# Optimization experiments

Hardware: AMD Instinct MI355X
Metric: run time of the kernel (lower is better)

The kernel has to match this reference:

```python
import jax, jax.numpy as jnp
import numpy as np

HEAD_NUM = 16
SCALE = 1.0 / np.sqrt(HEAD_NUM)  # source divides by sqrt(head_num), not head_dim
MASK_VAL = -10000000.0


def setup_inputs() -> dict:
    key = jax.random.key(0)
    kq, kk, kv = jax.random.split(key, 3)
    shape = (2, 16, 2048, 64)  # [B, H, L, D]
    Q = jax.random.normal(kq, shape, dtype=jnp.float32)
    K = jax.random.normal(kk, shape, dtype=jnp.float32)
    V = jax.random.normal(kv, shape, dtype=jnp.float32)
    return {"Q": Q, "K": K, "V": V}


def reference(Q, K, V):
    L = Q.shape[-2]
    # [B, H, L, M] attention logits, scaled by 1/sqrt(head_num)
    logits = jnp.einsum('bhld,bhmd->bhlm', Q, K) * SCALE
    # causal mask: strictly-upper triangle gets -1e7 (additive, as in source)
    mask = jnp.triu(jnp.ones((L, L), dtype=logits.dtype), 1) * MASK_VAL
    logits = logits + mask[None, None, :, :]
    weights = jax.nn.softmax(logits, axis=-1)
    return jnp.einsum('bhlm,bhmd->bhld', weights, V)
```

## Files before the change

### kernel.cpp

```cpp
#include <hip/hip_runtime.h>
#include <hip/hip_bf16.h>

#define BM 128
#define BN 64
#define HD 64
#define LQ 2048
#define SD 72

typedef __attribute__((ext_vector_type(8))) short short8;
typedef __attribute__((ext_vector_type(16))) float f32x16;

#define QSCALE 0.360673760222241f

static __device__ __forceinline__ unsigned pk2(float a, float b) {
    union { __hip_bfloat162 h2; unsigned u; } c;
    c.h2 = __float22bfloat162_rn(make_float2(a, b));
    return c.u;
}

__global__ __launch_bounds__(512, 4)
void fa_fwd(const float* __restrict__ Qg,
            const float* __restrict__ Kg,
            const float* __restrict__ Vg,
            float* __restrict__ Og) {
    __shared__ __align__(16) unsigned short lds[(2 * BN + 2 * HD) * SD];
    typedef unsigned short KT[BN][SD];
    typedef unsigned short VT[HD][SD];
    KT* sK  = (KT*)lds;
    VT* sVt = (VT*)(lds + 2 * BN * SD);

    const int t    = threadIdx.x;
    const int w    = t >> 6;
    const int lane = t & 63;
    const int h    = lane >> 5;
    const int l31  = lane & 31;
    const int qd   = lane >> 4;
    const int qg   = w & 3;
    const int kh   = w >> 2;

    const int bx  = blockIdx.x;
    const int idx = (bx >> 5) & 7;
    const int qt  = (bx & 256) ? idx : (15 - idx);
    const int bh  = bx & 31;
    const int q0  = qt * BM;

    const size_t base = (size_t)bh * (LQ * HD);
    const float* Qp = Qg + base + (size_t)q0 * HD;
    const float* Kp = Kg + base;
    const float* Vp = Vg + base;

    const int r0 = t >> 4;
    const int c4 = (t & 15) * 4;
    const int RA = w * 4;

    {
        unsigned short (*sQ)[SD] = (unsigned short (*)[SD])lds;
#pragma unroll
        for (int p = 0; p < 4; ++p) {
            const int r = p * 32 + r0;
            const float4 v = *(const float4*)(Qp + (size_t)r * HD + c4);
            uint2 u;
            u.x = pk2(v.x * QSCALE, v.y * QSCALE);
            u.y = pk2(v.z * QSCALE, v.w * QSCALE);
            *(uint2*)&sQ[r][c4] = u;
        }
    }
    __syncthreads();
    short8 qreg[4];
    {
        unsigned short (*sQ)[SD] = (unsigned short (*)[SD])lds;
#pragma unroll
        for (int ks = 0; ks < 4; ++ks)
            qreg[ks] = *(const short8*)&sQ[qg * 32 + l31][ks * 16 + h * 8];
    }
    __syncthreads();

    float4 kA, kB, vA, vB;

    auto issue = [&](int kv0) {
        kA = *(const float4*)(Kp + (size_t)(kv0 + r0) * HD + c4);
        kB = *(const float4*)(Kp + (size_t)(kv0 + 32 + r0) * HD + c4);
        vA = *(const float4*)(Vp + (size_t)(kv0 + RA + qd) * HD + c4);
        vB = *(const float4*)(Vp + (size_t)(kv0 + 32 + RA + qd) * HD + c4);
    };

    auto vstore = [&](float4 vf, int R, int buf) {
        float e0 = vf.x, e1 = vf.y, e2 = vf.z, e3 = vf.w;
        float s0 = (qd & 2) ? e0 : e2;
        float s1 = (qd & 2) ? e1 : e3;
        s0 = __shfl_xor(s0, 32); s1 = __shfl_xor(s1, 32);
        if (qd & 2) { e0 = s0; e1 = s1; } else { e2 = s0; e3 = s1; }
        s0 = (qd & 1) ? e0 : e1;
        s1 = (qd & 1) ? e2 : e3;
        s0 = __shfl_xor(s0, 16); s1 = __shfl_xor(s1, 16);
        if (qd & 1) { e0 = s0; e2 = s1; } else { e1 = s0; e3 = s1; }
        const int d   = c4 + qd;
        const int col = ((((R >> 3) ^ (d >> 3)) & 7) << 3) | (R & 7);
        uint2 u; u.x = pk2(e0, e1); u.y = pk2(e2, e3);
        *(uint2*)&sVt[buf][d][col] = u;
    };

    auto commit = [&](int buf) {
        { uint2 u; u.x = pk2(kA.x, kA.y); u.y = pk2(kA.z, kA.w);
          *(uint2*)&sK[buf][r0][c4] = u; }
        { uint2 u; u.x = pk2(kB.x, kB.y); u.y = pk2(kB.z, kB.w);
          *(uint2*)&sK[buf][32 + r0][c4] = u; }
        vstore(vA, RA, buf);
        vstore(vB, 32 + RA, buf);
    };

    f32x16 accO[2];
#pragma unroll
    for (int r = 0; r < 16; ++r) { accO[0][r] = 0.f; accO[1][r] = 0.f; }
    float lsum = 0.f;

    const int qminw = q0 + qg * 32;
    const int qmaxw = qminw + 31;
    const int n_it  = (q0 + BM) / BN;

    issue(0);
    commit(0);

    for (int it = 0; it < n_it; ++it) {
        const int kv0 = it * BN;
        const int buf = it & 1;
        __syncthreads();
        const bool more = (it + 1 < n_it);
        if (more) issue(kv0 + BN);

        if (kv0 + kh * 32 <= qmaxw) {
            f32x16 accS;
#pragma unroll
            for (int r = 0; r < 16; ++r) accS[r] = 0.f;
#pragma unroll
            for (int ks = 0; ks < 4; ++ks) {
                const short8 ak = *(const short8*)&sK[buf][kh * 32 + l31][ks * 16 + h * 8];
                accS = __builtin_amdgcn_mfma_f32_32x32x16_bf16(ak, qreg[ks], accS, 0, 0, 0);
            }

            if (kv0 + kh * 32 + 31 > qminw) {
                const int qrow = qminw + l31;
                const int kvb  = kv0 + kh * 32 + 4 * h;
#pragma unroll
                for (int r = 0; r < 16; ++r) {
                    const int kv = kvb + (r & 3) + 8 * (r >> 2);
                    if (kv > qrow) accS[r] = -1e30f;
                }
            }

#pragma unroll
            for (int r = 0; r < 16; ++r) {
                const float p = __builtin_amdgcn_exp2f(accS[r]);
                accS[r] = p;
                lsum += p;
            }

            short8 pf[2];
#pragma unroll
            for (int s = 0; s < 2; ++s) {
                const int rb = s * 8;
                const unsigned a0 = pk2(accS[rb + 0], accS[rb + 1]);
                const unsigned b0 = pk2(accS[rb + 4], accS[rb + 5]);
                const unsigned a1 = pk2(accS[rb + 2], accS[rb + 3]);
                const unsigned b1 = pk2(accS[rb + 6], accS[rb + 7]);
                const auto r02 = __builtin_amdgcn_permlane32_swap(a0, b0, 0, 0);
                const auto r13 = __builtin_amdgcn_permlane32_swap(a1, b1, 0, 0);
                union { unsigned u[4]; short8 s8; } pu;
                pu.u[0] = r02[0]; pu.u[1] = r13[0]; pu.u[2] = r02[1]; pu.u[3] = r13[1];
                pf[s] = pu.s8;
            }

#pragma unroll
            for (int s = 0; s < 2; ++s) {
                const int K0 = kh * 32 + s * 16 + h * 8;
#pragma unroll
                for (int dg = 0; dg < 2; ++dg) {
                    const int d   = dg * 32 + l31;
                    const int col = (((K0 >> 3) ^ (d >> 3)) & 7) << 3;
                    const short8 av = *(const short8*)&sVt[buf][d][col];
                    accO[dg] = __builtin_amdgcn_mfma_f32_32x32x16_bf16(av, pf[s], accO[dg], 0, 0, 0);
                }
            }
        }

        if (more) commit(buf ^ 1);
    }

    lsum += __shfl_xor(lsum, 32);
    __syncthreads();
    float* fx  = (float*)lds;
    float* fla = fx + 4 * 64 * 32;
    if (kh == 1) {
#pragma unroll
        for (int dg = 0; dg < 2; ++dg) {
#pragma unroll
            for (int r = 0; r < 16; ++r) {
                const int d = dg * 32 + (r & 3) + 8 * (r >> 2) + 4 * h;
                fx[(qg * 64 + d) * 32 + l31] = accO[dg][r];
            }
        }
        if (h == 0) fla[qg * 32 + l31] = lsum;
    }
    __syncthreads();
    if (kh == 0) {
        const float inv  = 1.0f / (lsum + fla[qg * 32 + l31]);
        const int   qrow = q0 + qg * 32 + l31;
        float* Op = Og + base + (size_t)qrow * HD;
#pragma unroll
        for (int dg = 0; dg < 2; ++dg) {
#pragma unroll
            for (int rq = 0; rq < 4; ++rq) {
                const int d = dg * 32 + 8 * rq + 4 * h;
                const float* fr = &fx[(qg * 64 + d) * 32 + l31];
                float4 o;
                o.x = (accO[dg][rq * 4 + 0] + fr[0])  * inv;
                o.y = (accO[dg][rq * 4 + 1] + fr[32]) * inv;
                o.z = (accO[dg][rq * 4 + 2] + fr[64]) * inv;
                o.w = (accO[dg][rq * 4 + 3] + fr[96]) * inv;
                *(float4*)(Op + d) = o;
            }
        }
    }
}

extern "C" void kernel_launch(void* const* d_in, const int* in_sizes, int n_in,
                              void* d_out, int out_size, void* d_ws, size_t ws_size,
                              hipStream_t stream) {
    const float* Q = (const float*)d_in[0];
    const float* K = (const float*)d_in[1];
    const float* V = (const float*)d_in[2];
    float* O = (float*)d_out;
    fa_fwd<<<dim3(512), dim3(512), 0, stream>>>(Q, K, V, O);
}
```

Before: 120.0 us.

## Halve query tile, prefetch K/V two tiles ahead, raise MFMA wave priority

Shrinks the query tile from 128 to 64 rows, so each block runs 4 waves and the grid doubles to 1024 blocks. Query tiles are remapped so heavy and light causal tiles are interleaved across the grid. The K/V pipeline now commits the next tile to LDS at the top of each iteration and issues global loads two tiles ahead, which should hide more memory latency at the cost of extra registers. MFMA sections are wrapped in s_setprio so matrix work is favoured over other waves; the smaller tile does mean each K/V tile is reused by fewer query rows.

```diff
diff --git a/kernel.cpp b/kernel.cpp
--- a/kernel.cpp
+++ b/kernel.cpp
@@ -1,7 +1,7 @@
 #include <hip/hip_runtime.h>
 #include <hip/hip_bf16.h>
 
-#define BM 128
+#define BM 64
 #define BN 64
 #define HD 64
 #define LQ 2048
@@ -18,7 +18,7 @@
     return c.u;
 }
 
-__global__ __launch_bounds__(512, 4)
+__global__ __launch_bounds__(256, 4)
 void fa_fwd(const float* __restrict__ Qg,
             const float* __restrict__ Kg,
             const float* __restrict__ Vg,
@@ -35,14 +35,15 @@
     const int h    = lane >> 5;
     const int l31  = lane & 31;
     const int qd   = lane >> 4;
-    const int qg   = w & 3;
-    const int kh   = w >> 2;
-
-    const int bx  = blockIdx.x;
-    const int idx = (bx >> 5) & 7;
-    const int qt  = (bx & 256) ? idx : (15 - idx);
-    const int bh  = bx & 31;
-    const int q0  = qt * BM;
+    const int qg   = w & 1;
+    const int kh   = w >> 1;
+
+    const int bx = blockIdx.x;
+    const int bh = bx & 31;
+    const int g  = bx >> 5;
+    const int gi = g & 7, gp = g >> 3;
+    const int qt = (gp & 1) ? ((gp & 2) * 8 + 15 - gi) : ((gp & 2) * 8 + gi);
+    const int q0 = qt * BM;
 
     const size_t base = (size_t)bh * (LQ * HD);
     const float* Qp = Qg + base + (size_t)q0 * HD;
@@ -57,7 +58,7 @@
         unsigned short (*sQ)[SD] = (unsigned short (*)[SD])lds;
 #pragma unroll
         for (int p = 0; p < 4; ++p) {
-            const int r = p * 32 + r0;
+            const int r = p * 16 + r0;
             const float4 v = *(const float4*)(Qp + (size_t)r * HD + c4);
             uint2 u;
             u.x = pk2(v.x * QSCALE, v.y * QSCALE);
@@ -75,13 +76,14 @@
     }
     __syncthreads();
 
-    float4 kA, kB, vA, vB;
+    float4 kR[4], vR[4];
 
     auto issue = [&](int kv0) {
-        kA = *(const float4*)(Kp + (size_t)(kv0 + r0) * HD + c4);
-        kB = *(const float4*)(Kp + (size_t)(kv0 + 32 + r0) * HD + c4);
-        vA = *(const float4*)(Vp + (size_t)(kv0 + RA + qd) * HD + c4);
-        vB = *(const float4*)(Vp + (size_t)(kv0 + 32 + RA + qd) * HD + c4);
+#pragma unroll
+        for (int p = 0; p < 4; ++p) {
+            kR[p] = *(const float4*)(Kp + (size_t)(kv0 + p * 16 + r0) * HD + c4);
+            vR[p] = *(const float4*)(Vp + (size_t)(kv0 + p * 16 + RA + qd) * HD + c4);
+        }
     };
 
     auto vstore = [&](float4 vf, int R, int buf) {
@@ -101,12 +103,14 @@
     };
 
     auto commit = [&](int buf) {
-        { uint2 u; u.x = pk2(kA.x, kA.y); u.y = pk2(kA.z, kA.w);
-          *(uint2*)&sK[buf][r0][c4] = u; }
-        { uint2 u; u.x = pk2(kB.x, kB.y); u.y = pk2(kB.z, kB.w);
-          *(uint2*)&sK[buf][32 + r0][c4] = u; }
-        vstore(vA, RA, buf);
-        vstore(vB, 32 + RA, buf);
+#pragma unroll
+        for (int p = 0; p < 4; ++p) {
+            uint2 u; u.x = pk2(kR[p].x, kR[p].y); u.y = pk2(kR[p].z, kR[p].w);
+            *(uint2*)&sK[buf][p * 16 + r0][c4] = u;
+        }
+#pragma unroll
+        for (int p = 0; p < 4; ++p)
+            vstore(vR[p], p * 16 + RA, buf);
     };
 
     f32x16 accO[2];
@@ -116,27 +120,30 @@
 
     const int qminw = q0 + qg * 32;
     const int qmaxw = qminw + 31;
-    const int n_it  = (q0 + BM) / BN;
+    const int n_it  = qt + 1;
 
     issue(0);
     commit(0);
+    if (n_it > 1) issue(BN);
 
     for (int it = 0; it < n_it; ++it) {
         const int kv0 = it * BN;
         const int buf = it & 1;
         __syncthreads();
-        const bool more = (it + 1 < n_it);
-        if (more) issue(kv0 + BN);
+        if (it + 1 < n_it) commit(buf ^ 1);
+        if (it + 2 < n_it) issue(kv0 + 2 * BN);
 
         if (kv0 + kh * 32 <= qmaxw) {
             f32x16 accS;
 #pragma unroll
             for (int r = 0; r < 16; ++r) accS[r] = 0.f;
+            __builtin_amdgcn_s_setprio(1);
 #pragma unroll
             for (int ks = 0; ks < 4; ++ks) {
                 const short8 ak = *(const short8*)&sK[buf][kh * 32 + l31][ks * 16 + h * 8];
                 accS = __builtin_amdgcn_mfma_f32_32x32x16_bf16(ak, qreg[ks], accS, 0, 0, 0);
             }
+            __builtin_amdgcn_s_setprio(0);
 
             if (kv0 + kh * 32 + 31 > qminw) {
                 const int qrow = qminw + l31;
@@ -170,6 +177,7 @@
                 pf[s] = pu.s8;
             }
 
+            __builtin_amdgcn_s_setprio(1);
 #pragma unroll
             for (int s = 0; s < 2; ++s) {
                 const int K0 = kh * 32 + s * 16 + h * 8;
@@ -181,15 +189,14 @@
                     accO[dg] = __builtin_amdgcn_mfma_f32_32x32x16_bf16(av, pf[s], accO[dg], 0, 0, 0);
                 }
             }
-        }
-
-        if (more) commit(buf ^ 1);
+            __builtin_amdgcn_s_setprio(0);
+        }
     }
 
     lsum += __shfl_xor(lsum, 32);
     __syncthreads();
     float* fx  = (float*)lds;
-    float* fla = fx + 4 * 64 * 32;
+    float* fla = fx + 2 * 64 * 32;
     if (kh == 1) {
 #pragma unroll
         for (int dg = 0; dg < 2; ++dg) {
@@ -230,5 +237,5 @@
     const float* K = (const float*)d_in[1];
     const float* V = (const float*)d_in[2];
     float* O = (float*)d_out;
-    fa_fwd<<<dim3(512), dim3(512), 0, stream>>>(Q, K, V, O);
+    fa_fwd<<<dim3(1024), dim3(256), 0, stream>>>(Q, K, V, O);
 }
```

New measurement: 165.3 us. 37.7% more time.

## Split KV range across block pairs with atomic last-arriver combine

Applied to the files above, without the earlier changes.

Adds a split-KV mode in which each (query tile, head) is handled by two blocks that each cover half of the causal KV range. Each block writes its unnormalized partial output and row sums to workspace, and the second block to arrive combines them and writes the output. This doubles the grid to raise parallelism and even out causal load imbalance, at the cost of a memset launch, extra global traffic and an atomic. It also wraps the MFMA sections in s_setprio hints. The split path runs only if a large enough workspace is supplied.

```diff
diff --git a/kernel.cpp b/kernel.cpp
--- a/kernel.cpp
+++ b/kernel.cpp
@@ -12,6 +12,11 @@
 
 #define QSCALE 0.360673760222241f
 
+#define WS_CNT_BYTES 2048
+#define WS_SLOT_F    8320
+#define WS_PAIR_F    (2 * WS_SLOT_F)
+#define WS_NEEDED    ((size_t)WS_CNT_BYTES + (size_t)512 * WS_PAIR_F * 4)
+
 static __device__ __forceinline__ unsigned pk2(float a, float b) {
     union { __hip_bfloat162 h2; unsigned u; } c;
     c.h2 = __float22bfloat162_rn(make_float2(a, b));
@@ -22,8 +27,11 @@
 void fa_fwd(const float* __restrict__ Qg,
             const float* __restrict__ Kg,
             const float* __restrict__ Vg,
-            float* __restrict__ Og) {
+            float* __restrict__ Og,
+            char* __restrict__ wsRaw,
+            int split) {
     __shared__ __align__(16) unsigned short lds[(2 * BN + 2 * HD) * SD];
+    __shared__ int sArr;
     typedef unsigned short KT[BN][SD];
     typedef unsigned short VT[HD][SD];
     KT* sK  = (KT*)lds;
@@ -38,11 +46,25 @@
     const int qg   = w & 3;
     const int kh   = w >> 2;
 
-    const int bx  = blockIdx.x;
-    const int idx = (bx >> 5) & 7;
-    const int qt  = (bx & 256) ? idx : (15 - idx);
-    const int bh  = bx & 31;
-    const int q0  = qt * BM;
+    const int bx = blockIdx.x;
+    int qt, bh, sp, pair;
+    if (split) {
+        qt   = 15 - (bx >> 6);
+        bh   = (bx >> 1) & 31;
+        sp   = bx & 1;
+        pair = bx >> 1;
+    } else {
+        const int idx = (bx >> 5) & 7;
+        qt   = (bx & 256) ? idx : (15 - idx);
+        bh   = bx & 31;
+        sp   = 0;
+        pair = 0;
+    }
+    const int q0 = qt * BM;
+
+    int it_lo, nloc;
+    if (split) { nloc = qt + 1; it_lo = sp * nloc; }
+    else       { nloc = 2 * qt + 2; it_lo = 0; }
 
     const size_t base = (size_t)bh * (LQ * HD);
     const float* Qp = Qg + base + (size_t)q0 * HD;
@@ -116,27 +138,28 @@
 
     const int qminw = q0 + qg * 32;
     const int qmaxw = qminw + 31;
-    const int n_it  = (q0 + BM) / BN;
-
-    issue(0);
+
+    issue(it_lo * BN);
     commit(0);
 
-    for (int it = 0; it < n_it; ++it) {
-        const int kv0 = it * BN;
-        const int buf = it & 1;
+    for (int i = 0; i < nloc; ++i) {
+        const int kv0 = (it_lo + i) * BN;
+        const int buf = i & 1;
         __syncthreads();
-        const bool more = (it + 1 < n_it);
+        const bool more = (i + 1 < nloc);
         if (more) issue(kv0 + BN);
 
         if (kv0 + kh * 32 <= qmaxw) {
             f32x16 accS;
 #pragma unroll
             for (int r = 0; r < 16; ++r) accS[r] = 0.f;
+            __builtin_amdgcn_s_setprio(1);
 #pragma unroll
             for (int ks = 0; ks < 4; ++ks) {
                 const short8 ak = *(const short8*)&sK[buf][kh * 32 + l31][ks * 16 + h * 8];
                 accS = __builtin_amdgcn_mfma_f32_32x32x16_bf16(ak, qreg[ks], accS, 0, 0, 0);
             }
+            __builtin_amdgcn_s_setprio(0);
 
             if (kv0 + kh * 32 + 31 > qminw) {
                 const int qrow = qminw + l31;
@@ -170,6 +193,7 @@
                 pf[s] = pu.s8;
             }
 
+            __builtin_amdgcn_s_setprio(1);
 #pragma unroll
             for (int s = 0; s < 2; ++s) {
                 const int K0 = kh * 32 + s * 16 + h * 8;
@@ -181,6 +205,7 @@
                     accO[dg] = __builtin_amdgcn_mfma_f32_32x32x16_bf16(av, pf[s], accO[dg], 0, 0, 0);
                 }
             }
+            __builtin_amdgcn_s_setprio(0);
         }
 
         if (more) commit(buf ^ 1);
@@ -202,10 +227,38 @@
         if (h == 0) fla[qg * 32 + l31] = lsum;
     }
     __syncthreads();
+
+    if (!split) {
+        if (kh == 0) {
+            const float inv  = 1.0f / (lsum + fla[qg * 32 + l31]);
+            const int   qrow = q0 + qg * 32 + l31;
+            float* Op = Og + base + (size_t)qrow * HD;
+#pragma unroll
+            for (int dg = 0; dg < 2; ++dg) {
+#pragma unroll
+                for (int rq = 0; rq < 4; ++rq) {
+                    const int d = dg * 32 + 8 * rq + 4 * h;
+                    const float* fr = &fx[(qg * 64 + d) * 32 + l31];
+                    float4 o;
+                    o.x = (accO[dg][rq * 4 + 0] + fr[0])  * inv;
+                    o.y = (accO[dg][rq * 4 + 1] + fr[32]) * inv;
+                    o.z = (accO[dg][rq * 4 + 2] + fr[64]) * inv;
+                    o.w = (accO[dg][rq * 4 + 3] + fr[96]) * inv;
+                    *(float4*)(Op + d) = o;
+                }
+            }
+        }
+        return;
+    }
+
+    int*   cnt = (int*)wsRaw;
+    float* wsF = (float*)(wsRaw + WS_CNT_BYTES);
+    float* slot = wsF + (size_t)pair * WS_PAIR_F + (size_t)sp * WS_SLOT_F;
+    float  psum = 0.f;
+    const int qr = qg * 32 + l31;
+
     if (kh == 0) {
-        const float inv  = 1.0f / (lsum + fla[qg * 32 + l31]);
-        const int   qrow = q0 + qg * 32 + l31;
-        float* Op = Og + base + (size_t)qrow * HD;
+        psum = lsum + fla[qr];
 #pragma unroll
         for (int dg = 0; dg < 2; ++dg) {
 #pragma unroll
@@ -213,10 +266,39 @@
                 const int d = dg * 32 + 8 * rq + 4 * h;
                 const float* fr = &fx[(qg * 64 + d) * 32 + l31];
                 float4 o;
-                o.x = (accO[dg][rq * 4 + 0] + fr[0])  * inv;
-                o.y = (accO[dg][rq * 4 + 1] + fr[32]) * inv;
-                o.z = (accO[dg][rq * 4 + 2] + fr[64]) * inv;
-                o.w = (accO[dg][rq * 4 + 3] + fr[96]) * inv;
+                o.x = accO[dg][rq * 4 + 0] + fr[0];
+                o.y = accO[dg][rq * 4 + 1] + fr[32];
+                o.z = accO[dg][rq * 4 + 2] + fr[64];
+                o.w = accO[dg][rq * 4 + 3] + fr[96];
+                *(float4*)(slot + (size_t)qr * HD + d) = o;
+            }
+        }
+        if (h == 0) slot[128 * HD + qr] = psum;
+    }
+    __threadfence();
+    __syncthreads();
+    if (t == 0)
+        sArr = __hip_atomic_fetch_add(&cnt[pair], 1,
+                                      __ATOMIC_ACQ_REL, __HIP_MEMORY_SCOPE_AGENT);
+    __syncthreads();
+
+    if (sArr == 1 && kh == 0) {
+        const float* pslot = wsF + (size_t)pair * WS_PAIR_F + (size_t)(sp ^ 1) * WS_SLOT_F;
+        const float inv  = 1.0f / (psum + pslot[128 * HD + qr]);
+        const int   qrow = q0 + qr;
+        float* Op = Og + base + (size_t)qrow * HD;
+#pragma unroll
+        for (int dg = 0; dg < 2; ++dg) {
+#pragma unroll
+            for (int rq = 0; rq < 4; ++rq) {
+                const int d = dg * 32 + 8 * rq + 4 * h;
+                const float* fr = &fx[(qg * 64 + d) * 32 + l31];
+                const float4 pp = *(const float4*)(pslot + (size_t)qr * HD + d);
+                float4 o;
+                o.x = (accO[dg][rq * 4 + 0] + fr[0]  + pp.x) * inv;
+                o.y = (accO[dg][rq * 4 + 1] + fr[32] + pp.y) * inv;
+                o.z = (accO[dg][rq * 4 + 2] + fr[64] + pp.z) * inv;
+                o.w = (accO[dg][rq * 4 + 3] + fr[96] + pp.w) * inv;
                 *(float4*)(Op + d) = o;
             }
         }
@@ -230,5 +312,10 @@
     const float* K = (const float*)d_in[1];
     const float* V = (const float*)d_in[2];
     float* O = (float*)d_out;
-    fa_fwd<<<dim3(512), dim3(512), 0, stream>>>(Q, K, V, O);
+    if (d_ws != nullptr && ws_size >= WS_NEEDED) {
+        hipMemsetAsync(d_ws, 0, WS_CNT_BYTES, stream);
+        fa_fwd<<<dim3(1024), dim3(512), 0, stream>>>(Q, K, V, O, (char*)d_ws, 1);
+    } else {
+        fa_fwd<<<dim3(512), dim3(512), 0, stream>>>(Q, K, V, O, nullptr, 0);
+    }
 }
```

Result: slower. 442.6 us (+268.8%).

## Pre-convert K/V to bf16 workspace and stream directly from global without LDS

Applied to the files above, without the earlier changes.

Adds a prep kernel that converts K to bf16 and V to a transposed bf16 layout in the workspace. A new main kernel then loads MFMA operands directly from global/L2, with no LDS staging or block barriers. Each wave owns 32 query rows and processes the full causal range, so the cross-wave reduction is gone. It also adds s_setprio around the MFMA blocks. The cost is an extra launch and extra global traffic, and direct global loads with no software prefetch may stall on latency. The old path stays as a fallback when no workspace is provided.

```diff
diff --git a/kernel.cpp b/kernel.cpp
--- a/kernel.cpp
+++ b/kernel.cpp
@@ -12,10 +12,180 @@
 
 #define QSCALE 0.360673760222241f
 
+#define WS_HALF  ((size_t)32 * 2048 * 64)
+#define WS_NEEDED (2 * WS_HALF * sizeof(unsigned short))
+
 static __device__ __forceinline__ unsigned pk2(float a, float b) {
     union { __hip_bfloat162 h2; unsigned u; } c;
     c.h2 = __float22bfloat162_rn(make_float2(a, b));
     return c.u;
+}
+
+__global__ __launch_bounds__(256)
+void prep(const float* __restrict__ Kg, const float* __restrict__ Vg,
+          unsigned short* __restrict__ Kb, unsigned short* __restrict__ Vt) {
+    __shared__ unsigned short sT[64][72];
+    const int t  = threadIdx.x;
+    const int bx = blockIdx.x;
+    const int bh = bx >> 5;
+    const int c  = bx & 31;
+    const size_t ibase = (size_t)bh * (LQ * HD) + (size_t)c * 64 * HD;
+    const int r  = t >> 4;
+    const int c4 = (t & 15) * 4;
+
+    unsigned short* Ko = Kb + ibase;
+#pragma unroll
+    for (int p = 0; p < 4; ++p) {
+        const int row = p * 16 + r;
+        const float4 v = *(const float4*)(Kg + ibase + (size_t)row * HD + c4);
+        uint2 u; u.x = pk2(v.x, v.y); u.y = pk2(v.z, v.w);
+        *(uint2*)&Ko[(size_t)row * HD + c4] = u;
+    }
+#pragma unroll
+    for (int p = 0; p < 4; ++p) {
+        const int row = p * 16 + r;
+        const float4 v = *(const float4*)(Vg + ibase + (size_t)row * HD + c4);
+        const unsigned u0 = pk2(v.x, v.y);
+        const unsigned u1 = pk2(v.z, v.w);
+        sT[c4 + 0][row] = (unsigned short)(u0 & 0xffff);
+        sT[c4 + 1][row] = (unsigned short)(u0 >> 16);
+        sT[c4 + 2][row] = (unsigned short)(u1 & 0xffff);
+        sT[c4 + 3][row] = (unsigned short)(u1 >> 16);
+    }
+    __syncthreads();
+    unsigned short* Vo = Vt + (size_t)bh * (HD * LQ) + (size_t)c * 64;
+    const int d = t >> 2, seg = t & 3;
+    *(uint4*)&Vo[(size_t)d * LQ + seg * 16]     = *(const uint4*)&sT[d][seg * 16];
+    *(uint4*)&Vo[(size_t)d * LQ + seg * 16 + 8] = *(const uint4*)&sT[d][seg * 16 + 8];
+}
+
+__global__ __launch_bounds__(256, 4)
+void fa_main(const float* __restrict__ Qg,
+             const unsigned short* __restrict__ Kb,
+             const unsigned short* __restrict__ Vt,
+             float* __restrict__ Og) {
+    const int t    = threadIdx.x;
+    const int w    = t >> 6;
+    const int lane = t & 63;
+    const int h    = lane >> 5;
+    const int l31  = lane & 31;
+
+    const int bx  = blockIdx.x;
+    const int idx = (bx >> 5) & 7;
+    const int qt  = (bx & 256) ? idx : (15 - idx);
+    const int bh  = bx & 31;
+    const int q0  = qt * BM;
+
+    const size_t base = (size_t)bh * (LQ * HD);
+    const unsigned short* Kh = Kb + base;
+    const unsigned short* Vh = Vt + base;
+
+    const int qrow = q0 + w * 32 + l31;
+    short8 qreg[4];
+    {
+        const float* Qrow = Qg + base + (size_t)qrow * HD;
+#pragma unroll
+        for (int ks = 0; ks < 4; ++ks) {
+            const float4 a = *(const float4*)(Qrow + ks * 16 + h * 8);
+            const float4 b = *(const float4*)(Qrow + ks * 16 + h * 8 + 4);
+            union { unsigned u[4]; short8 s8; } qu;
+            qu.u[0] = pk2(a.x * QSCALE, a.y * QSCALE);
+            qu.u[1] = pk2(a.z * QSCALE, a.w * QSCALE);
+            qu.u[2] = pk2(b.x * QSCALE, b.y * QSCALE);
+            qu.u[3] = pk2(b.z * QSCALE, b.w * QSCALE);
+            qreg[ks] = qu.s8;
+        }
+    }
+
+    f32x16 accO[2];
+#pragma unroll
+    for (int r = 0; r < 16; ++r) { accO[0][r] = 0.f; accO[1][r] = 0.f; }
+    float lsum = 0.f;
+
+    const int qminw = q0 + w * 32;
+    const int n_ch  = (qminw >> 5) + 1;
+
+    for (int ch = 0; ch < n_ch; ++ch) {
+        const int kv0 = ch * 32;
+
+        const unsigned short* kb = Kh + (size_t)(kv0 + l31) * HD + h * 8;
+        short8 ak[4];
+#pragma unroll
+        for (int ks = 0; ks < 4; ++ks)
+            ak[ks] = *(const short8*)(kb + ks * 16);
+        short8 av[2][2];
+#pragma unroll
+        for (int dg = 0; dg < 2; ++dg) {
+            const unsigned short* vb = Vh + (size_t)(dg * 32 + l31) * LQ + kv0 + h * 8;
+            av[0][dg] = *(const short8*)(vb);
+            av[1][dg] = *(const short8*)(vb + 16);
+        }
+
+        f32x16 accS;
+#pragma unroll
+        for (int r = 0; r < 16; ++r) accS[r] = 0.f;
+        __builtin_amdgcn_s_setprio(1);
+#pragma unroll
+        for (int ks = 0; ks < 4; ++ks)
+            accS = __builtin_amdgcn_mfma_f32_32x32x16_bf16(ak[ks], qreg[ks], accS, 0, 0, 0);
+        __builtin_amdgcn_s_setprio(0);
+
+        if (ch == n_ch - 1) {
+            const int kvb = kv0 + 4 * h;
+#pragma unroll
+            for (int r = 0; r < 16; ++r) {
+                const int kv = kvb + (r & 3) + 8 * (r >> 2);
+                if (kv > qrow) accS[r] = -1e30f;
+            }
+        }
+
+#pragma unroll
+        for (int r = 0; r < 16; ++r) {
+            const float p = __builtin_amdgcn_exp2f(accS[r]);
+            accS[r] = p;
+            lsum += p;
+        }
+
+        short8 pf[2];
+#pragma unroll
+        for (int s = 0; s < 2; ++s) {
+            const int rb = s * 8;
+            const unsigned a0 = pk2(accS[rb + 0], accS[rb + 1]);
+            const unsigned b0 = pk2(accS[rb + 4], accS[rb + 5]);
+            const unsigned a1 = pk2(accS[rb + 2], accS[rb + 3]);
+            const unsigned b1 = pk2(accS[rb + 6], accS[rb + 7]);
+            const auto r02 = __builtin_amdgcn_permlane32_swap(a0, b0, 0, 0);
+            const auto r13 = __builtin_amdgcn_permlane32_swap(a1, b1, 0, 0);
+            union { unsigned u[4]; short8 s8; } pu;
+            pu.u[0] = r02[0]; pu.u[1] = r13[0]; pu.u[2] = r02[1]; pu.u[3] = r13[1];
+            pf[s] = pu.s8;
+        }
+
+        __builtin_amdgcn_s_setprio(1);
+#pragma unroll
+        for (int s = 0; s < 2; ++s)
+#pragma unroll
+            for (int dg = 0; dg < 2; ++dg)
+                accO[dg] = __builtin_amdgcn_mfma_f32_32x32x16_bf16(av[s][dg], pf[s], accO[dg], 0, 0, 0);
+        __builtin_amdgcn_s_setprio(0);
+    }
+
+    lsum += __shfl_xor(lsum, 32);
+    const float inv = 1.0f / lsum;
+    float* Op = Og + base + (size_t)qrow * HD;
+#pragma unroll
+    for (int dg = 0; dg < 2; ++dg) {
+#pragma unroll
+        for (int rq = 0; rq < 4; ++rq) {
+            const int d = dg * 32 + 8 * rq + 4 * h;
+            float4 o;
+            o.x = accO[dg][rq * 4 + 0] * inv;
+            o.y = accO[dg][rq * 4 + 1] * inv;
+            o.z = accO[dg][rq * 4 + 2] * inv;
+            o.w = accO[dg][rq * 4 + 3] * inv;
+            *(float4*)(Op + d) = o;
+        }
+    }
 }
 
 __global__ __launch_bounds__(512, 4)
@@ -76,14 +246,12 @@
     __syncthreads();
 
     float4 kA, kB, vA, vB;
-
     auto issue = [&](int kv0) {
         kA = *(const float4*)(Kp + (size_t)(kv0 + r0) * HD + c4);
         kB = *(const float4*)(Kp + (size_t)(kv0 + 32 + r0) * HD + c4);
         vA = *(const float4*)(Vp + (size_t)(kv0 + RA + qd) * HD + c4);
         vB = *(const float4*)(Vp + (size_t)(kv0 + 32 + RA + qd) * HD + c4);
     };
-
     auto vstore = [&](float4 vf, int R, int buf) {
         float e0 = vf.x, e1 = vf.y, e2 = vf.z, e3 = vf.w;
         float s0 = (qd & 2) ? e0 : e2;
@@ -99,7 +267,6 @@
         uint2 u; u.x = pk2(e0, e1); u.y = pk2(e2, e3);
         *(uint2*)&sVt[buf][d][col] = u;
     };
-
     auto commit = [&](int buf) {
         { uint2 u; u.x = pk2(kA.x, kA.y); u.y = pk2(kA.z, kA.w);
           *(uint2*)&sK[buf][r0][c4] = u; }
@@ -132,11 +299,13 @@
             f32x16 accS;
 #pragma unroll
             for (int r = 0; r < 16; ++r) accS[r] = 0.f;
+            __builtin_amdgcn_s_setprio(1);
 #pragma unroll
             for (int ks = 0; ks < 4; ++ks) {
                 const short8 ak = *(const short8*)&sK[buf][kh * 32 + l31][ks * 16 + h * 8];
                 accS = __builtin_amdgcn_mfma_f32_32x32x16_bf16(ak, qreg[ks], accS, 0, 0, 0);
             }
+            __builtin_amdgcn_s_setprio(0);
 
             if (kv0 + kh * 32 + 31 > qminw) {
                 const int qrow = qminw + l31;
@@ -147,14 +316,12 @@
                     if (kv > qrow) accS[r] = -1e30f;
                 }
             }
-
 #pragma unroll
             for (int r = 0; r < 16; ++r) {
                 const float p = __builtin_amdgcn_exp2f(accS[r]);
                 accS[r] = p;
                 lsum += p;
             }
-
             short8 pf[2];
 #pragma unroll
             for (int s = 0; s < 2; ++s) {
@@ -169,7 +336,7 @@
                 pu.u[0] = r02[0]; pu.u[1] = r13[0]; pu.u[2] = r02[1]; pu.u[3] = r13[1];
                 pf[s] = pu.s8;
             }
-
+            __builtin_amdgcn_s_setprio(1);
 #pragma unroll
             for (int s = 0; s < 2; ++s) {
                 const int K0 = kh * 32 + s * 16 + h * 8;
@@ -181,6 +348,7 @@
                     accO[dg] = __builtin_amdgcn_mfma_f32_32x32x16_bf16(av, pf[s], accO[dg], 0, 0, 0);
                 }
             }
+            __builtin_amdgcn_s_setprio(0);
         }
 
         if (more) commit(buf ^ 1);
@@ -230,5 +398,12 @@
     const float* K = (const float*)d_in[1];
     const float* V = (const float*)d_in[2];
     float* O = (float*)d_out;
-    fa_fwd<<<dim3(512), dim3(512), 0, stream>>>(Q, K, V, O);
+    if (d_ws != nullptr && ws_size >= WS_NEEDED) {
+        unsigned short* Kb = (unsigned short*)d_ws;
+        unsigned short* Vt = Kb + WS_HALF;
+        prep<<<dim3(1024), dim3(256), 0, stream>>>(K, V, Kb, Vt);
+        fa_main<<<dim3(512), dim3(256), 0, stream>>>(Q, Kb, Vt, O);
+    } else {
+        fa_fwd<<<dim3(512), dim3(512), 0, stream>>>(Q, K, V, O);
+    }
 }
```

Result: slower. 155.2 us (+29.3%).
